# Optimization experiments

Hardware: AMD Instinct MI355X
Metric: run time of the kernel (lower is better)

The kernel has to match this reference:

```python
import jax, jax.numpy as jnp
import numpy as np

B, T, C, H = 2, 2048, 1024, 16
D = C // H  # head dim


def setup_inputs() -> dict:
    key = jax.random.key(0)
    k1, k2, k3 = jax.random.split(key, 3)
    x = jax.random.normal(k1, (B, T, C), dtype=jnp.float32)
    w_qkv = jax.random.normal(k2, (3 * C, C), dtype=jnp.float32) * (1.0 / np.sqrt(C))
    b_qkv = jnp.zeros((3 * C,), dtype=jnp.float32)
    w_proj = jax.random.normal(k3, (C, C), dtype=jnp.float32) * (1.0 / np.sqrt(C))
    b_proj = jnp.zeros((C,), dtype=jnp.float32)
    return {"x": x, "w_qkv": w_qkv, "b_qkv": b_qkv, "w_proj": w_proj, "b_proj": b_proj}


def reference(x, w_qkv, b_qkv, w_proj, b_proj):
    # torch Linear: y = x @ W^T + b
    qkv = jnp.einsum('btc,oc->bto', x, w_qkv) + b_qkv  # [B,T,3C]
    q, k, v = jnp.split(qkv, 3, axis=-1)
    # [B,T,C] -> [B,H,T,D]
    reshape = lambda t: t.reshape(B, T, H, D).transpose(0, 2, 1, 3)
    q, k, v = reshape(q), reshape(k), reshape(v)
    scale = 1.0 / jnp.sqrt(jnp.float32(C))  # NOTE: full C, as in source
    att = jnp.einsum('bhtd,bhsd->bhts', q, k) * scale  # [B,H,T,T]
    causal = jnp.tril(jnp.ones((T, T), dtype=bool))
    att = jnp.where(causal, att, -jnp.inf)
    att = jax.nn.softmax(att, axis=-1)
    y = jnp.einsum('bhts,bhsd->bhtd', att, v)  # [B,H,T,D]
    y = y.transpose(0, 2, 1, 3).reshape(B, T, C)
    return jnp.einsum('btc,oc->bto', y, w_proj) + b_proj
```

## Files before the change

kernel.cpp:

```cpp
#include <hip/hip_runtime.h>

#define DEVINL __device__ __forceinline__

typedef __attribute__((ext_vector_type(8))) short short8;
typedef __attribute__((ext_vector_type(4))) float f32x4;

DEVINL unsigned f2bf_u(float x) {
  union { float f; unsigned u; } v; v.f = x;
  unsigned r = v.u + 0x7FFF + ((v.u >> 16) & 1);
  return r >> 16;
}
DEVINL unsigned short f2bf(float x) { return (unsigned short)f2bf_u(x); }

DEVINL unsigned cvt_pk_bf16(float lo, float hi) {
  unsigned r;
  asm("v_cvt_pk_bf16_f32 %0, %1, %2" : "=v"(r) : "v"(lo), "v"(hi));
  return r;
}

#if __has_builtin(__builtin_amdgcn_exp2f)
#define EXP2(x) __builtin_amdgcn_exp2f(x)
#else
#define EXP2(x) exp2f(x)
#endif

DEVINL void gload_lds16(const void* g, void* l) {
  __builtin_amdgcn_global_load_lds(
      (const __attribute__((address_space(1))) unsigned int*)g,
      (__attribute__((address_space(3))) unsigned int*)l, 16, 0, 0);
}

DEVINL short8 as_s8(uint4 v) { union { uint4 u; short8 s; } c; c.u = v; return c.s; }
DEVINL f32x4 fzero() { f32x4 z = {0.f, 0.f, 0.f, 0.f}; return z; }

__global__ __launch_bounds__(256) void cvt3_kernel(
    const float4* __restrict__ x, const float4* __restrict__ wq,
    const float4* __restrict__ wp, ushort4* __restrict__ xo,
    ushort4* __restrict__ wqo, ushort4* __restrict__ wpo) {
  const int N1 = 1048576, N2 = 1835008, NT = 2097152;
  int i = blockIdx.x * blockDim.x + threadIdx.x;
  int stride = gridDim.x * blockDim.x;
  for (; i < NT; i += stride) {
    const float4* s; ushort4* d; int j;
    if (i < N1) { s = x; d = xo; j = i; }
    else if (i < N2) { s = wq; d = wqo; j = i - N1; }
    else { s = wp; d = wpo; j = i - N2; }
    float4 v = s[j];
    ushort4 o;
    o.x = f2bf(v.x); o.y = f2bf(v.y); o.z = f2bf(v.z); o.w = f2bf(v.w);
    d[j] = o;
  }
}

template <int MODE>
__global__ __launch_bounds__(256, 2) void gemm_bt(
    const ushort* __restrict__ A, const ushort* __restrict__ Bw,
    const float* __restrict__ bias,
    ushort* __restrict__ Qb, ushort* __restrict__ Kb, ushort* __restrict__ Vb,
    float* __restrict__ Out, int M, int N, int K) {
  __shared__ __align__(16) char smem[32768];
  char* ldsA = smem;
  char* ldsB = smem + 16384;

  int gx = gridDim.x;
  int nwg = gx * gridDim.y;
  int id = blockIdx.y * gx + blockIdx.x;
  int cpx = nwg >> 3;
  int sid = (id & 7) * cpx + (id >> 3);
  int bx = sid % gx, by = sid / gx;

  int m0 = by * 128, n0 = bx * 128;
  int t = threadIdx.x;
  int lane = t & 63, w = t >> 6;
  int q = lane & 15, g = lane >> 4;
  int wr = w >> 1, wc = w & 1;

  int Lrow[4], Lcol[4];
#pragma unroll
  for (int i = 0; i < 4; ++i) {
    int L = i * 4096 + t * 16;
    int row = L >> 7, c = L & 127;
    Lrow[i] = row;
    Lcol[i] = c ^ ((row & 7) << 4);
  }
  const char* Abase = (const char*)A + (size_t)m0 * K * 2;
  const char* Bbase = (const char*)Bw + (size_t)n0 * K * 2;

  f32x4 acc[4][4];
#pragma unroll
  for (int i = 0; i < 4; ++i)
#pragma unroll
    for (int j = 0; j < 4; ++j) acc[i][j] = fzero();

  for (int k0 = 0; k0 < K; k0 += 64) {
    __syncthreads();
#pragma unroll
    for (int i = 0; i < 4; ++i) {
      int L = i * 4096 + t * 16;
      gload_lds16(Abase + (size_t)Lrow[i] * (K * 2) + k0 * 2 + Lcol[i], ldsA + L);
    }
#pragma unroll
    for (int i = 0; i < 4; ++i) {
      int L = i * 4096 + t * 16;
      gload_lds16(Bbase + (size_t)Lrow[i] * (K * 2) + k0 * 2 + Lcol[i], ldsB + L);
    }
    __syncthreads();

    uint4 bf[2][4];
#pragma unroll
    for (int s = 0; s < 2; ++s)
#pragma unroll
      for (int nt = 0; nt < 4; ++nt) {
        int row = wc * 64 + nt * 16 + q;
        int addr = row * 128 + ((g * 16 + 64 * s) ^ ((row & 7) << 4));
        bf[s][nt] = *(const uint4*)(ldsB + addr);
      }
#pragma unroll
    for (int mt = 0; mt < 4; ++mt) {
      int row = wr * 64 + mt * 16 + q;
      int a0 = row * 128 + ((g * 16) ^ ((row & 7) << 4));
      int a1 = row * 128 + ((g * 16 + 64) ^ ((row & 7) << 4));
      uint4 af0 = *(const uint4*)(ldsA + a0);
      uint4 af1 = *(const uint4*)(ldsA + a1);
#pragma unroll
      for (int nt = 0; nt < 4; ++nt) {
        acc[mt][nt] = __builtin_amdgcn_mfma_f32_16x16x32_bf16(
            as_s8(af0), as_s8(bf[0][nt]), acc[mt][nt], 0, 0, 0);
        acc[mt][nt] = __builtin_amdgcn_mfma_f32_16x16x32_bf16(
            as_s8(af1), as_s8(bf[1][nt]), acc[mt][nt], 0, 0, 0);
      }
    }
  }

  if (MODE == 0) {
    __syncthreads();
    char* tile = smem + w * 8192;
    float bv[4];
#pragma unroll
    for (int nt = 0; nt < 4; ++nt) bv[nt] = bias[n0 + wc * 64 + nt * 16 + q];
#pragma unroll
    for (int mt = 0; mt < 4; ++mt)
#pragma unroll
      for (int nt = 0; nt < 4; ++nt)
#pragma unroll
        for (int r = 0; r < 4; ++r) {
          int row = mt * 16 + g * 4 + r;
          int bcol = ((nt * 16 + q) * 2) ^ ((row & 7) << 4);
          *(ushort*)(tile + row * 128 + bcol) = f2bf(acc[mt][nt][r] + bv[nt]);
        }
    int hs = (n0 + wc * 64) >> 6;
    int which = hs >> 4, h = hs & 15;
    ushort* dst = which == 0 ? Qb : (which == 1 ? Kb : Vb);
    int mrow0 = m0 + wr * 64;
    int b = mrow0 >> 11, tt0 = mrow0 & 2047;
    ushort* dbase = dst + (size_t)(b * 16 + h) * 131072 + (size_t)tt0 * 64;
#pragma unroll
    for (int p = 0; p < 8; ++p) {
      int row = p * 8 + (lane >> 3);
      int bcol = ((lane & 7) * 16) ^ ((row & 7) << 4);
      uint4 v = *(const uint4*)(tile + row * 128 + bcol);
      *(uint4*)(dbase + (size_t)row * 64 + (lane & 7) * 8) = v;
    }
  } else {
#pragma unroll
    for (int nt = 0; nt < 4; ++nt) {
      int ncol = n0 + wc * 64 + nt * 16 + q;
      float bv = bias[ncol];
#pragma unroll
      for (int mt = 0; mt < 4; ++mt)
#pragma unroll
        for (int r = 0; r < 4; ++r) {
          int m = m0 + wr * 64 + mt * 16 + g * 4 + r;
          Out[(size_t)m * N + ncol] = acc[mt][nt][r] + bv;
        }
    }
  }
}

__global__ __launch_bounds__(256) void vtrans(const ushort* __restrict__ V,
                                              ushort* __restrict__ Vt) {
  __shared__ ushort tile[64][72];
  int bh = blockIdx.y;
  int t0 = blockIdx.x * 64;
  int t = threadIdx.x;
#pragma unroll
  for (int it = 0; it < 2; ++it) {
    int row = it * 32 + (t >> 3);
    int c0 = (t & 7) * 8;
    uint4 v = *(const uint4*)(V + ((size_t)(bh * 2048 + t0 + row) * 64 + c0));
    *(uint4*)&tile[row][c0] = v;
  }
  __syncthreads();
#pragma unroll
  for (int it = 0; it < 2; ++it) {
    int d = t & 63;
    int tch = ((t >> 6) + 4 * it) * 8;
    ushort vals[8];
#pragma unroll
    for (int j = 0; j < 8; ++j) vals[j] = tile[tch + j][d];
    uint4 o;
    o.x = (unsigned)vals[0] | ((unsigned)vals[1] << 16);
    o.y = (unsigned)vals[2] | ((unsigned)vals[3] << 16);
    o.z = (unsigned)vals[4] | ((unsigned)vals[5] << 16);
    o.w = (unsigned)vals[6] | ((unsigned)vals[7] << 16);
    *(uint4*)(Vt + ((size_t)(bh * 64 + d) * 2048 + t0 + tch)) = o;
  }
}

__global__ __launch_bounds__(512, 1) void attn_kernel(
    const ushort* __restrict__ Q, const ushort* __restrict__ K,
    const ushort* __restrict__ Vt, ushort* __restrict__ Y) {
  __shared__ __align__(16) char smem[65536];
  const float C44 = 0.0450842298f;
  const float THR44 = 11.5415603f;
  int pidx = blockIdx.x;
  int bh = blockIdx.y;
  int t = threadIdx.x;
  int lane = t & 63, w = t >> 6;
  int q = lane & 15, g = lane >> 4;
  int wq = w & 3, half = w >> 2;
  int b = bh >> 4, hh = bh & 15;

  const char* Kc0 = (const char*)(K + (size_t)bh * 2048 * 64);
  const char* Vc0 = (const char*)(Vt + (size_t)bh * 64 * 2048);

  int krow[2], kcol[2], vrow[2], vcol[2];
#pragma unroll
  for (int i = 0; i < 2; ++i) {
    int L = i * 8192 + t * 16;
    krow[i] = L >> 7;
    kcol[i] = (L & 127) ^ ((krow[i] & 7) << 4);
    vrow[i] = L >> 8;
    vcol[i] = (L & 255) ^ ((vrow[i] & 7) << 4);
  }
  int offK[4][2], offV[4][2];
#pragma unroll
  for (int sub = 0; sub < 4; ++sub)
#pragma unroll
    for (int s = 0; s < 2; ++s) {
      offK[sub][s] = (half * 64 + sub * 16 + q) * 128 +
                     ((g * 16 + 64 * s) ^ ((q & 7) << 4));
      offV[sub][s] = 16384 + (sub * 16 + q) * 256 +
                     ((half * 128 + g * 16 + 64 * s) ^ ((q & 7) << 4));
    }

#pragma unroll 1
  for (int pass = 0; pass < 2; ++pass) {
    int qt = pass ? pidx : 31 - pidx;
    int nch = (qt >> 1) + 1;
    int qbase = qt * 64;
    int qrow0 = qbase + wq * 16;
    int qg = qrow0 + q;

    uint4 qf[2];
    {
      const ushort* Qrow = Q + ((size_t)bh * 2048 + qrow0 + q) * 64;
      qf[0] = *(const uint4*)(Qrow + g * 8);
      qf[1] = *(const uint4*)(Qrow + 32 + g * 8);
    }

    f32x4 oacc[4];
#pragma unroll
    for (int i = 0; i < 4; ++i) oacc[i] = fzero();
    float m_run = -1e30f;
    float l_run = 0.f;

#pragma unroll
    for (int i = 0; i < 2; ++i) {
      int L = i * 8192 + t * 16;
      gload_lds16(Kc0 + (size_t)krow[i] * 128 + kcol[i], smem + L);
      gload_lds16(Vc0 + (size_t)vrow[i] * 4096 + vcol[i], smem + 16384 + L);
    }
    __syncthreads();

    int cur = 0;
#pragma unroll 1
    for (int c = 0; c < nch; ++c) {
      int kv0 = c * 128;
      if (c + 1 < nch) {
        int kn = kv0 + 128;
        char* dstb = smem + (cur ^ 1) * 32768;
#pragma unroll
        for (int i = 0; i < 2; ++i) {
          int L = i * 8192 + t * 16;
          gload_lds16(Kc0 + (size_t)(kn + krow[i]) * 128 + kcol[i], dstb + L);
          gload_lds16(Vc0 + (size_t)vrow[i] * 4096 + (size_t)kn * 2 + vcol[i],
                      dstb + 16384 + L);
        }
      }
      const char* base = smem + cur * 32768;
      int kst = kv0 + half * 64;
      if (kst <= qrow0 + 15) {
        f32x4 sacc[4];
        __builtin_amdgcn_s_setprio(1);
#pragma unroll
        for (int sub = 0; sub < 4; ++sub) {
          sacc[sub] = fzero();
#pragma unroll
          for (int s = 0; s < 2; ++s)
            sacc[sub] = __builtin_amdgcn_mfma_f32_16x16x32_bf16(
                as_s8(*(const uint4*)(base + offK[sub][s])), as_s8(qf[s]),
                sacc[sub], 0, 0, 0);
        }
        __builtin_amdgcn_s_setprio(0);

        float sr[4][4];
        if (kst + 63 > qrow0) {
#pragma unroll
          for (int sub = 0; sub < 4; ++sub)
#pragma unroll
            for (int r = 0; r < 4; ++r) {
              int kv = kst + sub * 16 + g * 4 + r;
              sr[sub][r] = (kv > qg) ? -3e38f : sacc[sub][r];
            }
        } else {
#pragma unroll
          for (int sub = 0; sub < 4; ++sub)
#pragma unroll
            for (int r = 0; r < 4; ++r) sr[sub][r] = sacc[sub][r];
        }
        float ms[4];
#pragma unroll
        for (int sub = 0; sub < 4; ++sub)
          ms[sub] = fmaxf(fmaxf(sr[sub][0], sr[sub][1]),
                          fmaxf(sr[sub][2], sr[sub][3]));
        float mx44 = fmaxf(fmaxf(ms[0], ms[1]), fmaxf(ms[2], ms[3])) * C44;

        if (!__all(mx44 <= m_run + THR44)) {
          mx44 = fmaxf(mx44, __shfl_xor(mx44, 16));
          mx44 = fmaxf(mx44, __shfl_xor(mx44, 32));
          float mnew = fmaxf(m_run, mx44);
          float corr = EXP2(m_run - mnew);
          float cr[4];
#pragma unroll
          for (int r = 0; r < 4; ++r) cr[r] = __shfl(corr, g * 4 + r);
#pragma unroll
          for (int ds = 0; ds < 4; ++ds)
#pragma unroll
            for (int r = 0; r < 4; ++r) oacc[ds][r] *= cr[r];
          l_run *= corr;
          m_run = mnew;
        }

        float nm = -m_run;
        unsigned pk[4][2];
        float psum = 0.f;
#pragma unroll
        for (int sub = 0; sub < 4; ++sub) {
          float p0 = EXP2(__builtin_fmaf(sr[sub][0], C44, nm));
          float p1 = EXP2(__builtin_fmaf(sr[sub][1], C44, nm));
          float p2 = EXP2(__builtin_fmaf(sr[sub][2], C44, nm));
          float p3 = EXP2(__builtin_fmaf(sr[sub][3], C44, nm));
          psum += (p0 + p1) + (p2 + p3);
          pk[sub][0] = cvt_pk_bf16(p0, p1);
          pk[sub][1] = cvt_pk_bf16(p2, p3);
        }
        l_run += psum;

        uint4 pa[2];
#pragma unroll
        for (int h = 0; h < 2; ++h) {
          unsigned wrd[4];
#pragma unroll
          for (int j2 = 0; j2 < 4; ++j2) {
            int src = ((2 * (g & 1) + (j2 >> 1)) << 4) | q;
            unsigned lo = __shfl(pk[2 * h][j2 & 1], src);
            unsigned hi = __shfl(pk[2 * h + 1][j2 & 1], src);
            wrd[j2] = (g >> 1) ? hi : lo;
          }
          pa[h].x = wrd[0]; pa[h].y = wrd[1]; pa[h].z = wrd[2]; pa[h].w = wrd[3];
        }

        __builtin_amdgcn_s_setprio(1);
#pragma unroll
        for (int ds = 0; ds < 4; ++ds)
#pragma unroll
          for (int h = 0; h < 2; ++h)
            oacc[ds] = __builtin_amdgcn_mfma_f32_16x16x32_bf16(
                as_s8(pa[h]), as_s8(*(const uint4*)(base + offV[ds][h])),
                oacc[ds], 0, 0, 0);
        __builtin_amdgcn_s_setprio(0);
      }

      __syncthreads();
      cur ^= 1;
    }

    l_run += __shfl_xor(l_run, 16);
    l_run += __shfl_xor(l_run, 32);
    float* ob = (float*)smem + wq * 1024;
    float* mlb = (float*)(smem + 16384);
    if (half) {
#pragma unroll
      for (int ds = 0; ds < 4; ++ds)
#pragma unroll
        for (int r = 0; r < 4; ++r)
          ob[(g * 4 + r) * 64 + ds * 16 + q] = oacc[ds][r];
      if (g == 0) {
        mlb[wq * 32 + q] = m_run;
        mlb[wq * 32 + 16 + q] = l_run;
      }
    }
    __syncthreads();
    if (!half) {
#pragma unroll
      for (int r = 0; r < 4; ++r) {
        int row = g * 4 + r;
        float mA = __shfl(m_run, row);
        float lA = __shfl(l_run, row);
        float mB = mlb[wq * 32 + row];
        float lB = mlb[wq * 32 + 16 + row];
        float mS = fmaxf(mA, mB);
        float sA = EXP2(mA - mS), sB = EXP2(mB - mS);
        float linv = 1.0f / (lA * sA + lB * sB);
        sA *= linv; sB *= linv;
#pragma unroll
        for (int ds = 0; ds < 4; ++ds) {
          float vB = ob[row * 64 + ds * 16 + q];
          float yv = oacc[ds][r] * sA + vB * sB;
          Y[(size_t)(b * 2048 + qrow0 + row) * 1024 + hh * 64 + ds * 16 + q] =
              f2bf(yv);
        }
      }
    }
    __syncthreads();
  }
}

extern "C" void kernel_launch(void* const* d_in, const int* in_sizes, int n_in,
                              void* d_out, int out_size, void* d_ws, size_t ws_size,
                              hipStream_t stream) {
  const float* x = (const float*)d_in[0];
  const float* w_qkv = (const float*)d_in[1];
  const float* b_qkv = (const float*)d_in[2];
  const float* w_proj = (const float*)d_in[3];
  const float* b_proj = (const float*)d_in[4];
  float* out = (float*)d_out;
  char* ws = (char*)d_ws;
  const size_t MB = 1024 * 1024;
  ushort* xb    = (ushort*)(ws + 0 * MB);
  ushort* wqkvb = (ushort*)(ws + 8 * MB);
  ushort* wprojb= (ushort*)(ws + 14 * MB);
  ushort* Qb    = (ushort*)(ws + 16 * MB);
  ushort* Kb    = (ushort*)(ws + 24 * MB);
  ushort* Vb    = (ushort*)(ws + 32 * MB);
  ushort* Vt    = (ushort*)(ws + 40 * MB);
  ushort* Yb    = (ushort*)(ws + 48 * MB);

  cvt3_kernel<<<2048, 256, 0, stream>>>((const float4*)x, (const float4*)w_qkv,
                                        (const float4*)w_proj, (ushort4*)xb,
                                        (ushort4*)wqkvb, (ushort4*)wprojb);
  gemm_bt<0><<<dim3(24, 32), 256, 0, stream>>>(xb, wqkvb, b_qkv, Qb, Kb, Vb,
                                               nullptr, 4096, 3072, 1024);
  vtrans<<<dim3(32, 32), 256, 0, stream>>>(Vb, Vt);
  attn_kernel<<<dim3(16, 32), 512, 0, stream>>>(Qb, Kb, Vt, Yb);
  gemm_bt<1><<<dim3(8, 32), 256, 0, stream>>>(Yb, wprojb, b_proj, nullptr, nullptr,
                                              nullptr, out, 4096, 1024, 1024);
}
```

Baseline: 111.2 us.

## Fuse V transpose into QKV GEMM epilogue and remap blocks per XCD

The QKV GEMM epilogue now writes the V third directly in transposed [bh, d, t] layout using packed bf16 stores, so the separate vtrans kernel and its extra read/write pass over V are removed. Block-to-tile mapping in both GEMMs is changed to give each XCD a rectangular region of tiles, and the attention grid is flattened so each XCD handles whole heads. The aim is better L2 locality and one fewer launch. The cost is that the transposed V stores are strided 8-byte writes, which may coalesce poorly.

Result: faster. 101.2 us (-9.0%).

```diff
diff --git a/kernel.cpp b/kernel.cpp
--- a/kernel.cpp
+++ b/kernel.cpp
@@ -52,22 +52,22 @@
   }
 }
 
-template <int MODE>
+template <int MODE, int RX, int RY>
 __global__ __launch_bounds__(256, 2) void gemm_bt(
     const ushort* __restrict__ A, const ushort* __restrict__ Bw,
     const float* __restrict__ bias,
-    ushort* __restrict__ Qb, ushort* __restrict__ Kb, ushort* __restrict__ Vb,
+    ushort* __restrict__ Qb, ushort* __restrict__ Kb, ushort* __restrict__ Vt,
     float* __restrict__ Out, int M, int N, int K) {
   __shared__ __align__(16) char smem[32768];
   char* ldsA = smem;
   char* ldsB = smem + 16384;
 
   int gx = gridDim.x;
-  int nwg = gx * gridDim.y;
   int id = blockIdx.y * gx + blockIdx.x;
-  int cpx = nwg >> 3;
-  int sid = (id & 7) * cpx + (id >> 3);
-  int bx = sid % gx, by = sid / gx;
+  int xcd = id & 7, slot = id >> 3;
+  int rw = gx / RX, rh = gridDim.y / RY;
+  int bx = (xcd % RX) * rw + slot % rw;
+  int by = (xcd / RX) * rh + slot / rw;
 
   int m0 = by * 128, n0 = bx * 128;
   int t = threadIdx.x;
@@ -133,33 +133,51 @@
   }
 
   if (MODE == 0) {
-    __syncthreads();
-    char* tile = smem + w * 8192;
-    float bv[4];
-#pragma unroll
-    for (int nt = 0; nt < 4; ++nt) bv[nt] = bias[n0 + wc * 64 + nt * 16 + q];
-#pragma unroll
-    for (int mt = 0; mt < 4; ++mt)
-#pragma unroll
-      for (int nt = 0; nt < 4; ++nt)
-#pragma unroll
-        for (int r = 0; r < 4; ++r) {
-          int row = mt * 16 + g * 4 + r;
-          int bcol = ((nt * 16 + q) * 2) ^ ((row & 7) << 4);
-          *(ushort*)(tile + row * 128 + bcol) = f2bf(acc[mt][nt][r] + bv[nt]);
-        }
-    int hs = (n0 + wc * 64) >> 6;
-    int which = hs >> 4, h = hs & 15;
-    ushort* dst = which == 0 ? Qb : (which == 1 ? Kb : Vb);
     int mrow0 = m0 + wr * 64;
     int b = mrow0 >> 11, tt0 = mrow0 & 2047;
-    ushort* dbase = dst + (size_t)(b * 16 + h) * 131072 + (size_t)tt0 * 64;
-#pragma unroll
-    for (int p = 0; p < 8; ++p) {
-      int row = p * 8 + (lane >> 3);
-      int bcol = ((lane & 7) * 16) ^ ((row & 7) << 4);
-      uint4 v = *(const uint4*)(tile + row * 128 + bcol);
-      *(uint4*)(dbase + (size_t)row * 64 + (lane & 7) * 8) = v;
+    if (n0 >= 2048) {
+      int hs = (n0 + wc * 64) >> 6;
+      int h = hs & 15;
+      ushort* vb = Vt + ((size_t)(b * 16 + h) * 64) * 2048;
+#pragma unroll
+      for (int nt = 0; nt < 4; ++nt) {
+        int d = nt * 16 + q;
+        float bv = bias[n0 + wc * 64 + nt * 16 + q];
+#pragma unroll
+        for (int mt = 0; mt < 4; ++mt) {
+          uint2 o;
+          o.x = cvt_pk_bf16(acc[mt][nt][0] + bv, acc[mt][nt][1] + bv);
+          o.y = cvt_pk_bf16(acc[mt][nt][2] + bv, acc[mt][nt][3] + bv);
+          *(uint2*)(vb + (size_t)d * 2048 + tt0 + mt * 16 + g * 4) = o;
+        }
+      }
+    } else {
+      __syncthreads();
+      char* tile = smem + w * 8192;
+      float bv[4];
+#pragma unroll
+      for (int nt = 0; nt < 4; ++nt) bv[nt] = bias[n0 + wc * 64 + nt * 16 + q];
+#pragma unroll
+      for (int mt = 0; mt < 4; ++mt)
+#pragma unroll
+        for (int nt = 0; nt < 4; ++nt)
+#pragma unroll
+          for (int r = 0; r < 4; ++r) {
+            int row = mt * 16 + g * 4 + r;
+            int bcol = ((nt * 16 + q) * 2) ^ ((row & 7) << 4);
+            *(ushort*)(tile + row * 128 + bcol) = f2bf(acc[mt][nt][r] + bv[nt]);
+          }
+      int hs = (n0 + wc * 64) >> 6;
+      int which = hs >> 4, h = hs & 15;
+      ushort* dst = which == 0 ? Qb : Kb;
+      ushort* dbase = dst + (size_t)(b * 16 + h) * 131072 + (size_t)tt0 * 64;
+#pragma unroll
+      for (int p = 0; p < 8; ++p) {
+        int row = p * 8 + (lane >> 3);
+        int bcol = ((lane & 7) * 16) ^ ((row & 7) << 4);
+        uint4 v = *(const uint4*)(tile + row * 128 + bcol);
+        *(uint4*)(dbase + (size_t)row * 64 + (lane & 7) * 8) = v;
+      }
     }
   } else {
 #pragma unroll
@@ -174,36 +192,6 @@
           Out[(size_t)m * N + ncol] = acc[mt][nt][r] + bv;
         }
     }
-  }
-}
-
-__global__ __launch_bounds__(256) void vtrans(const ushort* __restrict__ V,
-                                              ushort* __restrict__ Vt) {
-  __shared__ ushort tile[64][72];
-  int bh = blockIdx.y;
-  int t0 = blockIdx.x * 64;
-  int t = threadIdx.x;
-#pragma unroll
-  for (int it = 0; it < 2; ++it) {
-    int row = it * 32 + (t >> 3);
-    int c0 = (t & 7) * 8;
-    uint4 v = *(const uint4*)(V + ((size_t)(bh * 2048 + t0 + row) * 64 + c0));
-    *(uint4*)&tile[row][c0] = v;
-  }
-  __syncthreads();
-#pragma unroll
-  for (int it = 0; it < 2; ++it) {
-    int d = t & 63;
-    int tch = ((t >> 6) + 4 * it) * 8;
-    ushort vals[8];
-#pragma unroll
-    for (int j = 0; j < 8; ++j) vals[j] = tile[tch + j][d];
-    uint4 o;
-    o.x = (unsigned)vals[0] | ((unsigned)vals[1] << 16);
-    o.y = (unsigned)vals[2] | ((unsigned)vals[3] << 16);
-    o.z = (unsigned)vals[4] | ((unsigned)vals[5] << 16);
-    o.w = (unsigned)vals[6] | ((unsigned)vals[7] << 16);
-    *(uint4*)(Vt + ((size_t)(bh * 64 + d) * 2048 + t0 + tch)) = o;
   }
 }
 
@@ -213,8 +201,10 @@
   __shared__ __align__(16) char smem[65536];
   const float C44 = 0.0450842298f;
   const float THR44 = 11.5415603f;
-  int pidx = blockIdx.x;
-  int bh = blockIdx.y;
+  int id = blockIdx.x;
+  int xcd = id & 7, slot = id >> 3;
+  int bh = xcd * 4 + (slot >> 4);
+  int pidx = slot & 15;
   int t = threadIdx.x;
   int lane = t & 63, w = t >> 6;
   int q = lane & 15, g = lane >> 4;
@@ -443,17 +433,16 @@
   ushort* wprojb= (ushort*)(ws + 14 * MB);
   ushort* Qb    = (ushort*)(ws + 16 * MB);
   ushort* Kb    = (ushort*)(ws + 24 * MB);
-  ushort* Vb    = (ushort*)(ws + 32 * MB);
   ushort* Vt    = (ushort*)(ws + 40 * MB);
   ushort* Yb    = (ushort*)(ws + 48 * MB);
 
   cvt3_kernel<<<2048, 256, 0, stream>>>((const float4*)x, (const float4*)w_qkv,
                                         (const float4*)w_proj, (ushort4*)xb,
                                         (ushort4*)wqkvb, (ushort4*)wprojb);
-  gemm_bt<0><<<dim3(24, 32), 256, 0, stream>>>(xb, wqkvb, b_qkv, Qb, Kb, Vb,
-                                               nullptr, 4096, 3072, 1024);
-  vtrans<<<dim3(32, 32), 256, 0, stream>>>(Vb, Vt);
-  attn_kernel<<<dim3(16, 32), 512, 0, stream>>>(Qb, Kb, Vt, Yb);
-  gemm_bt<1><<<dim3(8, 32), 256, 0, stream>>>(Yb, wprojb, b_proj, nullptr, nullptr,
-                                              nullptr, out, 4096, 1024, 1024);
-}
+  gemm_bt<0, 2, 4><<<dim3(24, 32), 256, 0, stream>>>(xb, wqkvb, b_qkv, Qb, Kb, Vt,
+                                                     nullptr, 4096, 3072, 1024);
+  attn_kernel<<<dim3(512), 512, 0, stream>>>(Qb, Kb, Vt, Yb);
+  gemm_bt<1, 1, 8><<<dim3(8, 32), 256, 0, stream>>>(Yb, wprojb, b_proj, nullptr,
+                                                    nullptr, nullptr, out, 4096,
+                                                    1024, 1024);
+}
```
